# Performance work log

Measured on AMD Instinct MI355X. Metric: run time of the kernel, lower is better.

Reference implementation:

```python
import jax, jax.numpy as jnp
import numpy as np

N = 16384   # rays
S = 128     # steps per ray (cfg.n_steps_fixed)
L = 10      # PE frequencies
EARLY_STOP_T = 1e-4


def _pe_encode(p):
    # p: [M, 3] -> [M, 3 + 6L]
    freqs = (2.0 ** jnp.arange(L, dtype=p.dtype))            # [L]
    ang = p[:, :, None] * freqs[None, None, :]               # [M,3,L]
    enc = jnp.concatenate([jnp.sin(ang), jnp.cos(ang)], axis=-1)  # [M,3,2L]
    return jnp.concatenate([p, enc.reshape(p.shape[0], -1)], axis=-1)


def setup_inputs() -> dict:
    key = jax.random.key(0)
    ks = jax.random.split(key, 16)
    d = {}
    d['orig_x'] = jax.random.normal(ks[0], (N,)) * 0.1
    d['orig_y'] = jax.random.normal(ks[1], (N,)) * 0.1
    d['orig_z'] = jax.random.normal(ks[2], (N,)) * 0.1
    dirs = jax.random.normal(ks[3], (N, 3))
    dirs = dirs / jnp.linalg.norm(dirs, axis=-1, keepdims=True)
    d['dir_x'], d['dir_y'], d['dir_z'] = dirs[:, 0], dirs[:, 1], dirs[:, 2]
    d['tmin'] = 2.0 + 0.1 * jax.random.uniform(ks[4], (N,))
    d['tmax'] = d['tmin'] + 4.0
    s1 = 1.0 / np.sqrt(63.0)
    s2 = 1.0 / np.sqrt(64.0)
    s3 = 1.0 / np.sqrt(16.0)
    d['W1'] = jax.random.normal(ks[5], (63, 64)) * s1
    d['b1'] = jnp.zeros((64,))
    d['W2'] = jax.random.normal(ks[6], (64, 64)) * s2
    d['b2'] = jnp.zeros((64,))
    d['W_out'] = jax.random.normal(ks[7], (64, 17)) * s2
    d['b_out'] = jnp.zeros((17,))
    d['W_rgb'] = jax.random.normal(ks[8], (16, 3)) * s3
    d['b_rgb'] = jnp.zeros((3,))
    return d


def reference(orig_x, orig_y, orig_z, dir_x, dir_y, dir_z, tmin, tmax,
              W1, b1, W2, b2, W_out, b_out, W_rgb, b_rgb):
    # --- _sample_fixed_steps ---
    t_lin = jnp.linspace(0.0, 1.0, S, dtype=jnp.float32)           # [S]
    t = tmin[:, None] + t_lin[None, :] * (tmax - tmin)[:, None]    # [N,S]
    dt = jax.lax.stop_gradient(jnp.mean(tmax - tmin)) / S          # scalar (.item() in torch)

    # --- positions [N,S,3] ---
    pos = jnp.stack([orig_x[:, None] + dir_x[:, None] * t,
                     orig_y[:, None] + dir_y[:, None] * t,
                     orig_z[:, None] + dir_z[:, None] * t], axis=-1)
    pos_flat = pos.reshape(-1, 3)

    # --- encoder + field MLP ---
    enc = _pe_encode(pos_flat)                                     # [NS,63]
    h = jax.nn.relu(enc @ W1 + b1)
    h = jax.nn.relu(h @ W2 + b2)
    out = h @ W_out + b_out                                        # [NS,17]
    sigma = jax.nn.relu(out[:, 0]).reshape(N, S)                   # density >= 0
    rgb_feat = out[:, 1:]

    # --- rgb head ---
    rgb_steps = jax.nn.sigmoid(rgb_feat @ W_rgb + b_rgb).reshape(N, S, 3)

    # --- alpha compositing with early ray termination ---
    alpha = 1.0 - jnp.exp(-sigma * dt)                             # [N,S]
    trans = jnp.cumprod(1.0 - alpha + 1e-10, axis=1)               # inclusive
    T = jnp.concatenate([jnp.ones((N, 1), alpha.dtype), trans[:, :-1]], axis=1)  # exclusive T_i
    keep = (T > EARLY_STOP_T).astype(alpha.dtype)                  # early_stop mask
    weights = T * alpha * keep                                     # [N,S]
    rgb_out = jnp.einsum('ns,nsc->nc', weights, rgb_steps)         # [N,3]
    T_out = trans[:, -1]                                           # final transmittance [N]
    return rgb_out, T_out
```

## Files before the change

### kernel.cpp

```cpp
#include <hip/hip_runtime.h>

typedef short short8 __attribute__((ext_vector_type(8)));
typedef float f32x4 __attribute__((ext_vector_type(4)));

#define NRAYS 16384
#define NS    128
#define INV2PI 0.15915494309189535f
#define LOG2E  1.4426950408889634f

#define F_B1  0
#define F_B2  64
#define F_BO4 128
#define F_NF  144

__device__ __forceinline__ float bf2f(unsigned short u){
  union { unsigned int i; float f; } v; v.i = ((unsigned int)u) << 16; return v.f;
}
__device__ __forceinline__ unsigned short f2bf(float f){
  union { unsigned int i; float f; } v; v.f = f;
  unsigned int i = v.i;
  unsigned int r = i + 0x7FFFu + ((i >> 16) & 1u);
  return (unsigned short)(r >> 16);
}
__device__ __forceinline__ unsigned cvtpk(float a, float b){
  unsigned r; asm("v_cvt_pk_bf16_f32 %0, %1, %2" : "=v"(r) : "v"(a), "v"(b));
  return r;
}
__device__ __forceinline__ float ldin(const void* p, int i, int isbf){
  return isbf ? bf2f(((const unsigned short*)p)[i]) : ((const float*)p)[i];
}
__device__ __forceinline__ int detect_bf(const void* tmn){
  const unsigned short* q = (const unsigned short*)tmn;
  int ok = 1;
  #pragma unroll
  for (int i = 0; i < 8; i++){
    float v = bf2f(q[2*i]);
    ok &= (v > 1.5f && v < 2.7f) ? 1 : 0;
  }
  return ok;
}
__device__ __forceinline__ float hw_fract(float x){ float r; asm("v_fract_f32 %0, %1":"=v"(r):"v"(x)); return r; }
__device__ __forceinline__ float hw_sin(float rev){ float f = hw_fract(rev); float r; asm("v_sin_f32 %0, %1":"=v"(r):"v"(f)); return r; }
__device__ __forceinline__ float hw_exp2(float x){ float r; asm("v_exp_f32 %0, %1":"=v"(r):"v"(x)); return r; }
__device__ __forceinline__ float hw_rcp(float x){ float r; asm("v_rcp_f32 %0, %1":"=v"(r):"v"(x)); return r; }
__device__ __forceinline__ float sigmoidf_hw(float a){
  return hw_rcp(1.f + hw_exp2(-a * LOG2E));
}
__device__ __forceinline__ float dpp_reduce_add(float x){
  float t;
  asm("v_add_f32 %0, %1, %1 row_shr:1 bound_ctrl:0"  : "=v"(t) : "v"(x));
  asm("v_add_f32 %0, %1, %1 row_shr:2 bound_ctrl:0"  : "=v"(x) : "v"(t));
  asm("v_add_f32 %0, %1, %1 row_shr:4 bound_ctrl:0"  : "=v"(t) : "v"(x));
  asm("v_add_f32 %0, %1, %1 row_shr:8 bound_ctrl:0"  : "=v"(x) : "v"(t));
  asm("v_add_f32 %0, %1, %1 row_bcast:15 row_mask:0xa bound_ctrl:0" : "=v"(t) : "v"(x));
  asm("v_add_f32 %0, %1, %1 row_bcast:31 row_mask:0xc bound_ctrl:0" : "=v"(x) : "v"(t));
  return x;
}

__global__ void nerf_prep(const void* __restrict__ tmn, const void* __restrict__ tmx,
                          const void* __restrict__ W1, const void* __restrict__ W2,
                          const void* __restrict__ Wout, const void* __restrict__ b1,
                          const void* __restrict__ b2, const void* __restrict__ bout,
                          const void* __restrict__ Wrgb, const void* __restrict__ brgb,
                          void* __restrict__ ws)
{
  const int tid = threadIdx.x;
  const int b   = blockIdx.x;
  const int isbf = detect_bf(tmn);
  unsigned short* w1f = (unsigned short*)ws;
  unsigned short* w2f = w1f + 4096;
  unsigned short* wof = w1f + 8192;
  float* wsf = (float*)((char*)ws + 18432);
  float* partials = wsf + F_NF;

  if (b < 64){
    const int i = b * 256 + tid;
    float d = ldin(tmx, i, isbf) - ldin(tmn, i, isbf);
    #pragma unroll
    for (int off = 32; off >= 1; off >>= 1) d += __shfl_down(d, off, 64);
    __shared__ float acc[4];
    if ((tid & 63) == 0) acc[tid >> 6] = d;
    __syncthreads();
    if (tid == 0) partials[b] = acc[0] + acc[1] + acc[2] + acc[3];
  } else if (b == 64){
    for (int e = tid; e < 4096; e += 256){
      int j = e & 7, n = (e >> 3) & 63, q = e >> 9;
      int k = q*8 + j;
      w1f[e] = (k < 63) ? f2bf(ldin(W1, k*64 + n, isbf)) : (unsigned short)0;
    }
  } else if (b == 65){
    for (int e = tid; e < 4096; e += 256){
      int j = e & 7, n = (e >> 3) & 63, q = e >> 9;
      int k = q*8 + j;
      w2f[e] = f2bf(ldin(W2, k*64 + n, isbf));
    }
  } else {
    for (int e = tid; e < 1024; e += 256){
      int j = e & 7, n = (e >> 3) & 15, q = e >> 7;
      int k = q*8 + j;
      float v = 0.f;
      if (n == 0) v = ldin(Wout, k*17 + 0, isbf);
      else if (n < 4){
        int c = n - 1;
        #pragma unroll
        for (int jj = 0; jj < 16; jj++)
          v += ldin(Wout, k*17 + 1 + jj, isbf) * ldin(Wrgb, jj*3 + c, isbf);
      }
      wof[e] = f2bf(v);
    }
    if (tid < 64){
      wsf[F_B1 + tid] = ldin(b1, tid, isbf);
      wsf[F_B2 + tid] = ldin(b2, tid, isbf);
    }
    if (tid >= 64 && tid < 67){
      int c = tid - 64;
      float v = ldin(brgb, c, isbf);
      #pragma unroll
      for (int jj = 0; jj < 16; jj++)
        v += ldin(bout, 1 + jj, isbf) * ldin(Wrgb, jj*3 + c, isbf);
      wsf[F_BO4 + 1 + c] = v;
    }
    if (tid == 67) wsf[F_BO4] = ldin(bout, 0, isbf);
  }
}

__global__ __launch_bounds__(128, 5)
void nerf_main(const void* __restrict__ ox, const void* __restrict__ oy,
               const void* __restrict__ oz, const void* __restrict__ dx,
               const void* __restrict__ dy, const void* __restrict__ dz,
               const void* __restrict__ tmn, const void* __restrict__ tmx,
               const void* __restrict__ ws, void* __restrict__ out)
{
  __shared__ __align__(16) char arena[16384];

  const int tid  = threadIdx.x;
  const int wid  = tid >> 6;
  const int lane = tid & 63;
  const int quad = lane >> 4;
  const int col  = lane & 15;
  const int m0   = wid * 64;
  const int isbf = detect_bf(tmn);

  const unsigned short* gW  = (const unsigned short*)ws;
  const float* wsf = (const float*)((const char*)ws + 18432);

  const int ray = blockIdx.x;
  unsigned short* sA = (unsigned short*)arena;

  {
    float tmin = ldin(tmn, ray, isbf);
    float tmax = ldin(tmx, ray, isbf);
    float t = tmin + ((float)tid * (1.0f/127.0f)) * (tmax - tmin);
    float p[3];
    p[0] = ldin(ox, ray, isbf) + ldin(dx, ray, isbf) * t;
    p[1] = ldin(oy, ray, isbf) + ldin(dy, ray, isbf) * t;
    p[2] = ldin(oz, ray, isbf) + ldin(dz, ray, isbf) * t;
    float enc[64];
    enc[0] = p[0]; enc[1] = p[1]; enc[2] = p[2]; enc[63] = 0.f;
    #pragma unroll
    for (int c = 0; c < 3; c++){
      float rv = p[c] * INV2PI;
      const int bix = 3 + c*20;
      float sv = hw_sin(rv);
      float cv = hw_sin(rv + 0.25f);
      enc[bix] = sv; enc[bix+10] = cv;
      #pragma unroll
      for (int l = 1; l < 10; l++){
        float s2 = 2.f*sv*cv;
        float c2 = cv*cv - sv*sv;
        enc[bix+l] = s2; enc[bix+10+l] = c2;
        sv = s2; cv = c2;
      }
    }
    #pragma unroll
    for (int q = 0; q < 8; q++){
      uint4 w;
      w.x = cvtpk(enc[q*8+0], enc[q*8+1]);
      w.y = cvtpk(enc[q*8+2], enc[q*8+3]);
      w.z = cvtpk(enc[q*8+4], enc[q*8+5]);
      w.w = cvtpk(enc[q*8+6], enc[q*8+7]);
      *(uint4*)(sA + (q*128 + tid)*8) = w;
    }
  }

  #pragma unroll
  for (int layer = 0; layer < 2; layer++){
    const unsigned short* Wf = gW + layer*4096;
    const float* bptr = wsf + (layer ? F_B2 : F_B1);
    short8 wf[8];
    f32x4 bia[4];
    #pragma unroll
    for (int nt = 0; nt < 4; nt++){
      wf[nt*2]   = *(const short8*)(Wf + ((quad    )*64 + nt*16 + col)*8);
      wf[nt*2+1] = *(const short8*)(Wf + ((quad + 4)*64 + nt*16 + col)*8);
      bia[nt]    = *(const f32x4*)(bptr + nt*16 + quad*4);
    }
    #pragma unroll
    for (int mt = 0; mt < 4; mt++){
      const int m = m0 + mt*16 + col;
      short8 h0 = *(const short8*)(sA + ((quad    )*128 + m)*8);
      short8 h1 = *(const short8*)(sA + ((quad + 4)*128 + m)*8);
      #pragma unroll
      for (int nt = 0; nt < 4; nt++){
        f32x4 c = bia[nt];
        c = __builtin_amdgcn_mfma_f32_16x16x32_bf16(wf[nt*2],   h0, c, 0, 0, 0);
        c = __builtin_amdgcn_mfma_f32_16x16x32_bf16(wf[nt*2+1], h1, c, 0, 0, 0);
        uint2 pw;
        pw.x = cvtpk(fmaxf(c[0], 0.f), fmaxf(c[1], 0.f));
        pw.y = cvtpk(fmaxf(c[2], 0.f), fmaxf(c[3], 0.f));
        const int qw = nt*2 + (quad >> 1);
        *(uint2*)(sA + (qw*128 + m)*8 + (quad & 1)*4) = pw;
      }
    }
  }

  {
    const unsigned short* Wo = gW + 8192;
    short8 wo0 = *(const short8*)(Wo + ((quad    )*16 + col)*8);
    short8 wo1 = *(const short8*)(Wo + ((quad + 4)*16 + col)*8);
    f32x4 bo4 = {0.f, 0.f, 0.f, 0.f};
    if (quad == 0) bo4 = *(const f32x4*)(wsf + F_BO4);
    float* Of = (float*)arena;
    #pragma unroll
    for (int mt = 0; mt < 4; mt++){
      const int m = m0 + mt*16 + col;
      short8 h0 = *(const short8*)(sA + ((quad    )*128 + m)*8);
      short8 h1 = *(const short8*)(sA + ((quad + 4)*128 + m)*8);
      f32x4 c = bo4;
      c = __builtin_amdgcn_mfma_f32_16x16x32_bf16(wo0, h0, c, 0, 0, 0);
      c = __builtin_amdgcn_mfma_f32_16x16x32_bf16(wo1, h1, c, 0, 0, 0);
      if (quad == 0) *(f32x4*)(Of + m*4) = c;
    }
  }
  __syncthreads();

  float pv = wsf[F_NF + lane];
  pv = dpp_reduce_add(pv);
  const float dtv = __builtin_amdgcn_readlane(pv, 63) *
                    (1.0f / ((float)NRAYS * (float)NS));

  const float* Of = (const float*)arena;
  float* aux = (float*)(arena + 4096);
  f32x4 o = *(const f32x4*)(Of + tid*4);
  float sigma = fmaxf(o[0], 0.f);
  float e2 = hw_exp2(-sigma * dtv * LOG2E);
  float alpha = 1.f - e2;
  float rc = sigmoidf_hw(o[1]);
  float gc = sigmoidf_hw(o[2]);
  float bc = sigmoidf_hw(o[3]);

  float v = e2 + 1e-10f;
  #pragma unroll
  for (int off = 1; off < 64; off <<= 1){
    float tt = __shfl_up(v, off, 64);
    v = (lane >= off) ? v * tt : v;
  }
  if (wid == 0 && lane == 63) aux[0] = v;
  __syncthreads();
  const float P0 = aux[0];
  float vfull = wid ? v * P0 : v;
  float tp = __shfl_up(vfull, 1, 64);
  float T = (lane == 0) ? (wid ? P0 : 1.f) : tp;
  float w = (T > 1e-4f) ? T * alpha : 0.f;
  float sr = dpp_reduce_add(w * rc);
  float sg = dpp_reduce_add(w * gc);
  float sb = dpp_reduce_add(w * bc);
  if (lane == 63){
    aux[4 + wid*4] = sr; aux[5 + wid*4] = sg; aux[6 + wid*4] = sb;
    if (wid == 1) aux[12] = vfull;
  }
  __syncthreads();
  if (tid == 0){
    float rr = aux[4] + aux[8], gg = aux[5] + aux[9], bb = aux[6] + aux[10];
    float Tout = aux[12];
    if (isbf){
      unsigned short* ob = (unsigned short*)out;
      ob[ray*3 + 0]     = f2bf(rr);
      ob[ray*3 + 1]     = f2bf(gg);
      ob[ray*3 + 2]     = f2bf(bb);
      ob[3*NRAYS + ray] = f2bf(Tout);
    } else {
      float* of = (float*)out;
      of[ray*3 + 0]     = rr;
      of[ray*3 + 1]     = gg;
      of[ray*3 + 2]     = bb;
      of[3*NRAYS + ray] = Tout;
    }
  }
}

extern "C" void kernel_launch(void* const* d_in, const int* in_sizes, int n_in,
                              void* d_out, int out_size, void* d_ws, size_t ws_size,
                              hipStream_t stream)
{
  nerf_prep<<<67, 256, 0, stream>>>(d_in[6], d_in[7], d_in[8], d_in[10], d_in[12],
                                    d_in[9], d_in[11], d_in[13], d_in[14], d_in[15],
                                    d_ws);
  nerf_main<<<NRAYS, 128, 0, stream>>>(d_in[0], d_in[1], d_in[2], d_in[3],
                                       d_in[4], d_in[5], d_in[6], d_in[7],
                                       d_ws, d_out);
}
```

Before: 147.4 us.

## Split MLP over four waves per ray and precompute dt in prep kernel

The main kernel now launches 256 threads per ray instead of 128, so each of four waves handles 32 samples of the MLP rather than two waves handling 64. Only the first 128 threads do encoding and compositing, and a barrier is added after encoding. The prep kernel collapses the 64 partial-sum blocks into a single block that reduces the full dt sum and stores dt and the dtype flag. The main kernel then reads these instead of re-detecting the dtype and reducing partials per block. The intent is more parallelism across waves and less redundant per-block work, at the cost of idle threads in the scalar phases, an extra barrier, and a serial single-block reduction in prep.

Measured after the change: 241.4 us. 1.64x slower.

```diff
diff --git a/kernel.cpp b/kernel.cpp
--- a/kernel.cpp
+++ b/kernel.cpp
@@ -8,10 +8,11 @@
 #define INV2PI 0.15915494309189535f
 #define LOG2E  1.4426950408889634f
 
-#define F_B1  0
-#define F_B2  64
-#define F_BO4 128
-#define F_NF  144
+#define F_B1   0
+#define F_B2   64
+#define F_BO4  128
+#define F_DT   132
+#define F_ISBF 133
 
 __device__ __forceinline__ float bf2f(unsigned short u){
   union { unsigned int i; float f; } v; v.i = ((unsigned int)u) << 16; return v.f;
@@ -71,30 +72,20 @@
   unsigned short* w2f = w1f + 4096;
   unsigned short* wof = w1f + 8192;
   float* wsf = (float*)((char*)ws + 18432);
-  float* partials = wsf + F_NF;
-
-  if (b < 64){
-    const int i = b * 256 + tid;
-    float d = ldin(tmx, i, isbf) - ldin(tmn, i, isbf);
-    #pragma unroll
-    for (int off = 32; off >= 1; off >>= 1) d += __shfl_down(d, off, 64);
-    __shared__ float acc[4];
-    if ((tid & 63) == 0) acc[tid >> 6] = d;
-    __syncthreads();
-    if (tid == 0) partials[b] = acc[0] + acc[1] + acc[2] + acc[3];
-  } else if (b == 64){
+
+  if (b == 0){
     for (int e = tid; e < 4096; e += 256){
       int j = e & 7, n = (e >> 3) & 63, q = e >> 9;
       int k = q*8 + j;
       w1f[e] = (k < 63) ? f2bf(ldin(W1, k*64 + n, isbf)) : (unsigned short)0;
     }
-  } else if (b == 65){
+  } else if (b == 1){
     for (int e = tid; e < 4096; e += 256){
       int j = e & 7, n = (e >> 3) & 63, q = e >> 9;
       int k = q*8 + j;
       w2f[e] = f2bf(ldin(W2, k*64 + n, isbf));
     }
-  } else {
+  } else if (b == 2){
     for (int e = tid; e < 1024; e += 256){
       int j = e & 7, n = (e >> 3) & 15, q = e >> 7;
       int k = q*8 + j;
@@ -121,10 +112,24 @@
       wsf[F_BO4 + 1 + c] = v;
     }
     if (tid == 67) wsf[F_BO4] = ldin(bout, 0, isbf);
-  }
-}
-
-__global__ __launch_bounds__(128, 5)
+  } else {
+    float s = 0.f;
+    for (int i = tid; i < NRAYS; i += 256)
+      s += ldin(tmx, i, isbf) - ldin(tmn, i, isbf);
+    #pragma unroll
+    for (int off = 32; off >= 1; off >>= 1) s += __shfl_down(s, off, 64);
+    __shared__ float acc[4];
+    if ((tid & 63) == 0) acc[tid >> 6] = s;
+    __syncthreads();
+    if (tid == 0){
+      wsf[F_DT] = (acc[0] + acc[1] + acc[2] + acc[3]) *
+                  (1.0f / ((float)NRAYS * (float)NS));
+      ((int*)wsf)[F_ISBF] = isbf;
+    }
+  }
+}
+
+__global__ __launch_bounds__(256, 8)
 void nerf_main(const void* __restrict__ ox, const void* __restrict__ oy,
                const void* __restrict__ oz, const void* __restrict__ dx,
                const void* __restrict__ dy, const void* __restrict__ dz,
@@ -138,16 +143,17 @@
   const int lane = tid & 63;
   const int quad = lane >> 4;
   const int col  = lane & 15;
-  const int m0   = wid * 64;
-  const int isbf = detect_bf(tmn);
+  const int m0   = wid * 32;
 
   const unsigned short* gW  = (const unsigned short*)ws;
   const float* wsf = (const float*)((const char*)ws + 18432);
+  const int   isbf = ((const int*)wsf)[F_ISBF];
+  const float dtv  = wsf[F_DT];
 
   const int ray = blockIdx.x;
   unsigned short* sA = (unsigned short*)arena;
 
-  {
+  if (tid < 128){
     float tmin = ldin(tmn, ray, isbf);
     float tmax = ldin(tmx, ray, isbf);
     float t = tmin + ((float)tid * (1.0f/127.0f)) * (tmax - tmin);
@@ -182,6 +188,7 @@
       *(uint4*)(sA + (q*128 + tid)*8) = w;
     }
   }
+  __syncthreads();
 
   #pragma unroll
   for (int layer = 0; layer < 2; layer++){
@@ -196,7 +203,7 @@
       bia[nt]    = *(const f32x4*)(bptr + nt*16 + quad*4);
     }
     #pragma unroll
-    for (int mt = 0; mt < 4; mt++){
+    for (int mt = 0; mt < 2; mt++){
       const int m = m0 + mt*16 + col;
       short8 h0 = *(const short8*)(sA + ((quad    )*128 + m)*8);
       short8 h1 = *(const short8*)(sA + ((quad + 4)*128 + m)*8);
@@ -222,7 +229,7 @@
     if (quad == 0) bo4 = *(const f32x4*)(wsf + F_BO4);
     float* Of = (float*)arena;
     #pragma unroll
-    for (int mt = 0; mt < 4; mt++){
+    for (int mt = 0; mt < 2; mt++){
       const int m = m0 + mt*16 + col;
       short8 h0 = *(const short8*)(sA + ((quad    )*128 + m)*8);
       short8 h1 = *(const short8*)(sA + ((quad + 4)*128 + m)*8);
@@ -234,40 +241,40 @@
   }
   __syncthreads();
 
-  float pv = wsf[F_NF + lane];
-  pv = dpp_reduce_add(pv);
-  const float dtv = __builtin_amdgcn_readlane(pv, 63) *
-                    (1.0f / ((float)NRAYS * (float)NS));
-
   const float* Of = (const float*)arena;
   float* aux = (float*)(arena + 4096);
-  f32x4 o = *(const f32x4*)(Of + tid*4);
-  float sigma = fmaxf(o[0], 0.f);
-  float e2 = hw_exp2(-sigma * dtv * LOG2E);
-  float alpha = 1.f - e2;
-  float rc = sigmoidf_hw(o[1]);
-  float gc = sigmoidf_hw(o[2]);
-  float bc = sigmoidf_hw(o[3]);
-
-  float v = e2 + 1e-10f;
-  #pragma unroll
-  for (int off = 1; off < 64; off <<= 1){
-    float tt = __shfl_up(v, off, 64);
-    v = (lane >= off) ? v * tt : v;
-  }
-  if (wid == 0 && lane == 63) aux[0] = v;
+  float v = 0.f, alpha = 0.f, rc = 0.f, gc = 0.f, bc = 0.f;
+  if (tid < 128){
+    f32x4 o = *(const f32x4*)(Of + tid*4);
+    float sigma = fmaxf(o[0], 0.f);
+    float e2 = hw_exp2(-sigma * dtv * LOG2E);
+    alpha = 1.f - e2;
+    rc = sigmoidf_hw(o[1]);
+    gc = sigmoidf_hw(o[2]);
+    bc = sigmoidf_hw(o[3]);
+
+    v = e2 + 1e-10f;
+    #pragma unroll
+    for (int off = 1; off < 64; off <<= 1){
+      float tt = __shfl_up(v, off, 64);
+      v = (lane >= off) ? v * tt : v;
+    }
+    if (wid == 0 && lane == 63) aux[0] = v;
+  }
   __syncthreads();
-  const float P0 = aux[0];
-  float vfull = wid ? v * P0 : v;
-  float tp = __shfl_up(vfull, 1, 64);
-  float T = (lane == 0) ? (wid ? P0 : 1.f) : tp;
-  float w = (T > 1e-4f) ? T * alpha : 0.f;
-  float sr = dpp_reduce_add(w * rc);
-  float sg = dpp_reduce_add(w * gc);
-  float sb = dpp_reduce_add(w * bc);
-  if (lane == 63){
-    aux[4 + wid*4] = sr; aux[5 + wid*4] = sg; aux[6 + wid*4] = sb;
-    if (wid == 1) aux[12] = vfull;
+  if (tid < 128){
+    const float P0 = aux[0];
+    float vfull = wid ? v * P0 : v;
+    float tp = __shfl_up(vfull, 1, 64);
+    float T = (lane == 0) ? (wid ? P0 : 1.f) : tp;
+    float w = (T > 1e-4f) ? T * alpha : 0.f;
+    float sr = dpp_reduce_add(w * rc);
+    float sg = dpp_reduce_add(w * gc);
+    float sb = dpp_reduce_add(w * bc);
+    if (lane == 63){
+      aux[4 + wid*4] = sr; aux[5 + wid*4] = sg; aux[6 + wid*4] = sb;
+      if (wid == 1) aux[12] = vfull;
+    }
   }
   __syncthreads();
   if (tid == 0){
@@ -293,10 +300,10 @@
                               void* d_out, int out_size, void* d_ws, size_t ws_size,
                               hipStream_t stream)
 {
-  nerf_prep<<<67, 256, 0, stream>>>(d_in[6], d_in[7], d_in[8], d_in[10], d_in[12],
-                                    d_in[9], d_in[11], d_in[13], d_in[14], d_in[15],
-                                    d_ws);
-  nerf_main<<<NRAYS, 128, 0, stream>>>(d_in[0], d_in[1], d_in[2], d_in[3],
+  nerf_prep<<<4, 256, 0, stream>>>(d_in[6], d_in[7], d_in[8], d_in[10], d_in[12],
+                                   d_in[9], d_in[11], d_in[13], d_in[14], d_in[15],
+                                   d_ws);
+  nerf_main<<<NRAYS, 256, 0, stream>>>(d_in[0], d_in[1], d_in[2], d_in[3],
                                        d_in[4], d_in[5], d_in[6], d_in[7],
                                        d_ws, d_out);
 }
```
